# Optimization experiments

Measured on AMD Instinct MI355X. Metric: run time of the kernel, lower is better.

The kernel has to match this reference:

```python
import jax, jax.numpy as jnp
import numpy as np

N_NODES = 100000

def setup_inputs() -> dict:
    key = jax.random.key(0)
    k1, k2, k3, k4 = jax.random.split(key, 4)
    feat = jax.random.normal(k1, (N_NODES, 128), dtype=jnp.float32)
    weight = jax.random.normal(k2, (128, 64), dtype=jnp.float32) * 0.05
    src = jax.random.randint(k3, (600000,), 0, N_NODES, dtype=jnp.int64)
    dst = jax.random.randint(k4, (600000,), 0, N_NODES, dtype=jnp.int64)
    return {"feat": feat, "weight": weight, "src": src, "dst": dst}

def reference(feat, weight, src, dst):
    n = feat.shape[0]
    ones = jnp.ones(src.shape[0], dtype=jnp.float32)
    # out-degree of source nodes (edges leave src), in-degree of dst nodes
    out_deg = jnp.clip(jax.ops.segment_sum(ones, src, num_segments=n), 1.0)
    in_deg = jnp.clip(jax.ops.segment_sum(ones, dst, num_segments=n), 1.0)
    norm_src = (out_deg ** -0.5)[:, None]   # [N,1]
    norm_dst = (in_deg ** -0.5)[:, None]    # [N,1]
    # in_feats (128) > out_feats (64): project first, then aggregate
    h = jnp.matmul(feat, weight) * norm_src              # [N, 64]
    msgs = h[src]                                        # [E, 64] gather
    rst = jax.ops.segment_sum(msgs, dst, num_segments=n)  # [N, 64] scatter-sum
    rst = rst * norm_dst
    return rst
```

## Files before the change

kernel.cpp:

```cpp
#include <hip/hip_runtime.h>
#include <hip/hip_fp16.h>

#define IN_F 128
#define OUT_F 64
#define NB    256
#define BSH   9
#define CAP   3840
#define CHUNK 2048
#define KPF  136
#define KPW  144

using short8  = __attribute__((ext_vector_type(8))) short;
using float4v = __attribute__((ext_vector_type(4))) float;

static __device__ inline unsigned short f2bf(float x) {
    union { float f; unsigned u; } v; v.f = x;
    unsigned r = (v.u + 0x7fffu + ((v.u >> 16) & 1u)) >> 16;
    return (unsigned short)r;
}

__global__ __launch_bounds__(256) void bin_gemm_kernel(
    const int* __restrict__ src, const int* __restrict__ dst,
    int* __restrict__ gcur_d, int* __restrict__ gcur_s,
    unsigned* __restrict__ bkt_d, unsigned short* __restrict__ bkt_s,
    int E, int nbin,
    const float* __restrict__ feat, const float* __restrict__ W,
    __half* __restrict__ h, int n)
{
    __shared__ union {
        struct { int hd[NB]; int hs[NB]; int based[NB]; int bases[NB]; } bin;
        struct { unsigned short Fh[128 * KPF]; unsigned short Wt[64 * KPW]; } gm;
    } smem;

    const int tid = threadIdx.x;

    if (blockIdx.x < (unsigned)nbin) {
        const int e0 = blockIdx.x * CHUNK;

        smem.bin.hd[tid] = 0; smem.bin.hs[tid] = 0;
        __syncthreads();

        int sv[8], dv[8];
        #pragma unroll
        for (int j = 0; j < 8; ++j) {
            int i = e0 + j * 256 + tid;
            if (i < E) { sv[j] = src[i]; dv[j] = dst[i]; }
            else       { sv[j] = -1;     dv[j] = -1; }
        }
        #pragma unroll
        for (int j = 0; j < 8; ++j) {
            if (dv[j] >= 0) {
                atomicAdd(&smem.bin.hd[dv[j] >> BSH], 1);
                atomicAdd(&smem.bin.hs[sv[j] >> BSH], 1);
            }
        }
        __syncthreads();

        int cd = smem.bin.hd[tid], cs = smem.bin.hs[tid];
        smem.bin.based[tid] = cd ? atomicAdd(&gcur_d[tid], cd) : 0;
        smem.bin.bases[tid] = cs ? atomicAdd(&gcur_s[tid], cs) : 0;
        smem.bin.hd[tid] = 0; smem.bin.hs[tid] = 0;
        __syncthreads();

        #pragma unroll
        for (int j = 0; j < 8; ++j) {
            if (dv[j] >= 0) {
                int bd = dv[j] >> BSH;
                int pd = atomicAdd(&smem.bin.hd[bd], 1) + smem.bin.based[bd];
                if (pd < CAP)
                    bkt_d[(size_t)bd * CAP + pd] =
                        (unsigned)sv[j] | ((unsigned)(dv[j] & 511) << 17);
                int bs = sv[j] >> BSH;
                int ps = atomicAdd(&smem.bin.hs[bs], 1) + smem.bin.bases[bs];
                if (ps < CAP) bkt_s[(size_t)bs * CAP + ps] = (unsigned short)(sv[j] & 511);
            }
        }
        return;
    }

    unsigned short* Fh = smem.gm.Fh;
    unsigned short* Wt = smem.gm.Wt;
    const int row0 = (blockIdx.x - nbin) * 128;

    {
        const float4* W4 = (const float4*)W;
        #pragma unroll
        for (int it = 0; it < 8; ++it) {
            int i4 = it * 256 + tid;
            int k  = i4 >> 4;
            int c4 = (i4 & 15) * 4;
            float4 wv = W4[i4];
            Wt[(c4 + 0) * KPW + k] = f2bf(wv.x);
            Wt[(c4 + 1) * KPW + k] = f2bf(wv.y);
            Wt[(c4 + 2) * KPW + k] = f2bf(wv.z);
            Wt[(c4 + 3) * KPW + k] = f2bf(wv.w);
        }
    }
    {
        const float4* F4 = (const float4*)feat;
        #pragma unroll
        for (int it = 0; it < 16; ++it) {
            int i4 = it * 256 + tid;
            int r  = i4 >> 5;
            int c4 = (i4 & 31) * 4;
            int gr = row0 + r; if (gr >= n) gr = n - 1;
            float4 v = F4[(long)gr * 32 + (i4 & 31)];
            ushort4 u;
            u.x = f2bf(v.x); u.y = f2bf(v.y); u.z = f2bf(v.z); u.w = f2bf(v.w);
            *(ushort4*)&Fh[r * KPF + c4] = u;
        }
    }
    __syncthreads();

    const int w  = tid >> 6;
    const int l  = tid & 63;
    const int ml = l & 15;
    const int q  = l >> 4;

    float4v acc[2][4];
    #pragma unroll
    for (int rt = 0; rt < 2; ++rt)
        #pragma unroll
        for (int ct = 0; ct < 4; ++ct)
            acc[rt][ct] = (float4v){0.f, 0.f, 0.f, 0.f};

    #pragma unroll
    for (int ks = 0; ks < 4; ++ks) {
        const int ko = ks * 32 + q * 8;
        short8 a0 = *(const short8*)&Fh[(w * 32 +  0 + ml) * KPF + ko];
        short8 a1 = *(const short8*)&Fh[(w * 32 + 16 + ml) * KPF + ko];
        short8 b0 = *(const short8*)&Wt[( 0 + ml) * KPW + ko];
        short8 b1 = *(const short8*)&Wt[(16 + ml) * KPW + ko];
        short8 b2 = *(const short8*)&Wt[(32 + ml) * KPW + ko];
        short8 b3 = *(const short8*)&Wt[(48 + ml) * KPW + ko];
        acc[0][0] = __builtin_amdgcn_mfma_f32_16x16x32_bf16(a0, b0, acc[0][0], 0, 0, 0);
        acc[0][1] = __builtin_amdgcn_mfma_f32_16x16x32_bf16(a0, b1, acc[0][1], 0, 0, 0);
        acc[0][2] = __builtin_amdgcn_mfma_f32_16x16x32_bf16(a0, b2, acc[0][2], 0, 0, 0);
        acc[0][3] = __builtin_amdgcn_mfma_f32_16x16x32_bf16(a0, b3, acc[0][3], 0, 0, 0);
        acc[1][0] = __builtin_amdgcn_mfma_f32_16x16x32_bf16(a1, b0, acc[1][0], 0, 0, 0);
        acc[1][1] = __builtin_amdgcn_mfma_f32_16x16x32_bf16(a1, b1, acc[1][1], 0, 0, 0);
        acc[1][2] = __builtin_amdgcn_mfma_f32_16x16x32_bf16(a1, b2, acc[1][2], 0, 0, 0);
        acc[1][3] = __builtin_amdgcn_mfma_f32_16x16x32_bf16(a1, b3, acc[1][3], 0, 0, 0);
    }

    #pragma unroll
    for (int rt = 0; rt < 2; ++rt) {
        #pragma unroll
        for (int reg = 0; reg < 4; ++reg) {
            int row = row0 + w * 32 + rt * 16 + q * 4 + reg;
            if (row < n) {
                #pragma unroll
                for (int ct = 0; ct < 4; ++ct)
                    h[(long)row * OUT_F + ct * 16 + ml] = __float2half(acc[rt][ct][reg]);
            }
        }
    }
}

__global__ __launch_bounds__(256) void csr_kernel(
    const unsigned* __restrict__ bkt_d, const unsigned short* __restrict__ bkt_s,
    const int* __restrict__ gcur_d, const int* __restrict__ gcur_s,
    int2* __restrict__ off_deg, int* __restrict__ ebuf, int* __restrict__ outdeg, int n)
{
    __shared__ int hist[512], curs[512], hist_s[512];
    __shared__ int wsum[4];
    const int b = blockIdx.x, tid = threadIdx.x;
    const int cnt   = min(gcur_d[b], CAP);
    const int cnt_s = min(gcur_s[b], CAP);

    hist[tid] = 0; hist[tid + 256] = 0;
    hist_s[tid] = 0; hist_s[tid + 256] = 0;
    __syncthreads();

    unsigned rec[15];
    int nrec = 0;
    for (int i = tid; i < cnt; i += 256) {
        unsigned e = bkt_d[(size_t)b * CAP + i];
        rec[nrec++] = e;
        atomicAdd(&hist[e >> 17], 1);
    }
    for (int i = tid; i < cnt_s; i += 256)
        atomicAdd(&hist_s[bkt_s[(size_t)b * CAP + i]], 1);
    __syncthreads();

    int a0 = hist[2 * tid], a1 = hist[2 * tid + 1];
    int psum = a0 + a1;
    const int lane = tid & 63, w = tid >> 6;
    int x = psum;
    #pragma unroll
    for (int off = 1; off < 64; off <<= 1) {
        int y = __shfl_up(x, off);
        if (lane >= off) x += y;
    }
    if (lane == 63) wsum[w] = x;
    __syncthreads();
    int wbase = 0;
    for (int i = 0; i < w; ++i) wbase += wsum[i];
    int excl = x + wbase - psum;
    curs[2 * tid]     = excl;
    curs[2 * tid + 1] = excl + a0;
    off_deg[b * 512 + 2 * tid]     = make_int2(b * CAP + excl,      a0);
    off_deg[b * 512 + 2 * tid + 1] = make_int2(b * CAP + excl + a0, a1);
    __syncthreads();

    for (int j = 0; j < nrec; ++j) {
        unsigned e = rec[j];
        int p = atomicAdd(&curs[e >> 17], 1);
        if (p < CAP) ebuf[b * CAP + p] = (int)(e & 0x1FFFFu);
    }

    int node = b * 512 + tid;
    if (node < n) outdeg[node] = hist_s[tid];
    node += 256;
    if (node < n) outdeg[node] = hist_s[tid + 256];
}

__global__ __launch_bounds__(256) void gather_kernel(
    const int* __restrict__ ebuf, const int2* __restrict__ off_deg,
    const int* __restrict__ outdeg,
    const __half* __restrict__ h, float* __restrict__ out, int n)
{
    int d = blockIdx.x * 4 + (threadIdx.x >> 6);
    int l = threadIdx.x & 63;
    int o = l >> 3;
    int t = l & 7;
    if (d >= n) return;
    int2 od = off_deg[d];
    int beg = od.x, m = od.y, end = od.x + od.y;
    float a0 = 0.f, a1 = 0.f, a2 = 0.f, a3 = 0.f;
    float a4 = 0.f, a5 = 0.f, a6 = 0.f, a7 = 0.f;
    for (int j = beg + o; j < end; j += 8) {
        int s = ebuf[j];
        float ns = rsqrtf(fmaxf((float)outdeg[s], 1.0f));
        union { uint4 u; __half2 h2[4]; } P;
        P.u = *(const uint4*)&h[(long)s * OUT_F + 8 * t];
        float2 f0 = __half22float2(P.h2[0]);
        float2 f1 = __half22float2(P.h2[1]);
        float2 f2 = __half22float2(P.h2[2]);
        float2 f3 = __half22float2(P.h2[3]);
        a0 = fmaf(f0.x, ns, a0); a1 = fmaf(f0.y, ns, a1);
        a2 = fmaf(f1.x, ns, a2); a3 = fmaf(f1.y, ns, a3);
        a4 = fmaf(f2.x, ns, a4); a5 = fmaf(f2.y, ns, a5);
        a6 = fmaf(f3.x, ns, a6); a7 = fmaf(f3.y, ns, a7);
    }
    #pragma unroll
    for (int mask = 8; mask <= 32; mask <<= 1) {
        a0 += __shfl_xor(a0, mask); a1 += __shfl_xor(a1, mask);
        a2 += __shfl_xor(a2, mask); a3 += __shfl_xor(a3, mask);
        a4 += __shfl_xor(a4, mask); a5 += __shfl_xor(a5, mask);
        a6 += __shfl_xor(a6, mask); a7 += __shfl_xor(a7, mask);
    }
    if (o == 0) {
        float nd = rsqrtf(fmaxf((float)m, 1.0f));
        float4 v0 = make_float4(a0 * nd, a1 * nd, a2 * nd, a3 * nd);
        float4 v1 = make_float4(a4 * nd, a5 * nd, a6 * nd, a7 * nd);
        *(float4*)&out[(long)d * OUT_F + 8 * t]     = v0;
        *(float4*)&out[(long)d * OUT_F + 8 * t + 4] = v1;
    }
}

extern "C" void kernel_launch(void* const* d_in, const int* in_sizes, int n_in,
                              void* d_out, int out_size, void* d_ws, size_t ws_size,
                              hipStream_t stream) {
    const float* feat = (const float*)d_in[0];
    const float* W    = (const float*)d_in[1];
    const int*   src  = (const int*)d_in[2];
    const int*   dst  = (const int*)d_in[3];
    float* out = (float*)d_out;

    const int n = in_sizes[0] / IN_F;
    const int E = in_sizes[2];

    char* wsb = (char*)d_ws;
    int* gcur_d = (int*)wsb;
    int* gcur_s = gcur_d + NB;
    int* outdeg = gcur_s + NB;
    size_t pos = (((size_t)(2 * NB + n)) * 4 + 15) & ~(size_t)15;
    int2* off_deg = (int2*)(wsb + pos);
    pos = (pos + (size_t)NB * 512 * 8 + 15) & ~(size_t)15;
    int* ebuf = (int*)(wsb + pos);
    pos = (pos + (size_t)NB * CAP * 4 + 15) & ~(size_t)15;
    unsigned* bkt_d = (unsigned*)(wsb + pos);
    pos = (pos + (size_t)NB * CAP * 4 + 15) & ~(size_t)15;
    unsigned short* bkt_s = (unsigned short*)(wsb + pos);
    pos = (pos + (size_t)NB * CAP * 2 + 15) & ~(size_t)15;
    __half* h = (__half*)(wsb + pos);

    hipMemsetAsync(gcur_d, 0, 2 * NB * sizeof(int), stream);

    const int nbin  = (E + CHUNK - 1) / CHUNK;
    const int ngemm = (n + 127) / 128;

    bin_gemm_kernel<<<nbin + ngemm, 256, 0, stream>>>(src, dst, gcur_d, gcur_s,
                                                      bkt_d, bkt_s, E, nbin,
                                                      feat, W, h, n);
    csr_kernel<<<NB, 256, 0, stream>>>(bkt_d, bkt_s, gcur_d, gcur_s,
                                       off_deg, ebuf, outdeg, n);
    gather_kernel<<<(n + 3) / 4, 256, 0, stream>>>(ebuf, off_deg, outdeg, h, out, n);
}
```

Before: 155.9 us.

## Replace CSR build and per-node gather with per-bucket LDS atomic accumulation

Drops the CSR construction (histogram, scan, edge scatter into ebuf) and the per-destination gather kernel. Instead, each of 256 blocks processes its destination bucket directly and accumulates messages into a 512x65 float LDS tile with shared-memory atomics, then normalizes and writes out. Out-degree counting moves to a small separate kernel. This removes a global write and read pass plus a kernel's worth of work, at the cost of LDS atomic contention and only 256 blocks with ~133KB LDS each, which limits occupancy to one block per CU.

Measured after the change: 383.2 us. 146% more time.

```diff
diff --git a/kernel.cpp b/kernel.cpp
--- a/kernel.cpp
+++ b/kernel.cpp
@@ -9,6 +9,7 @@
 #define CHUNK 2048
 #define KPF  136
 #define KPW  144
+#define APITCH 65
 
 using short8  = __attribute__((ext_vector_type(8))) short;
 using float4v = __attribute__((ext_vector_type(4))) float;
@@ -157,80 +158,51 @@
     }
 }
 
-__global__ __launch_bounds__(256) void csr_kernel(
-    const unsigned* __restrict__ bkt_d, const unsigned short* __restrict__ bkt_s,
-    const int* __restrict__ gcur_d, const int* __restrict__ gcur_s,
-    int2* __restrict__ off_deg, int* __restrict__ ebuf, int* __restrict__ outdeg, int n)
+__global__ __launch_bounds__(256) void outdeg_kernel(
+    const unsigned short* __restrict__ bkt_s, const int* __restrict__ gcur_s,
+    int* __restrict__ outdeg, int n)
 {
-    __shared__ int hist[512], curs[512], hist_s[512];
-    __shared__ int wsum[4];
+    __shared__ int hs[512];
     const int b = blockIdx.x, tid = threadIdx.x;
-    const int cnt   = min(gcur_d[b], CAP);
     const int cnt_s = min(gcur_s[b], CAP);
 
-    hist[tid] = 0; hist[tid + 256] = 0;
-    hist_s[tid] = 0; hist_s[tid + 256] = 0;
-    __syncthreads();
-
-    unsigned rec[15];
-    int nrec = 0;
-    for (int i = tid; i < cnt; i += 256) {
-        unsigned e = bkt_d[(size_t)b * CAP + i];
-        rec[nrec++] = e;
-        atomicAdd(&hist[e >> 17], 1);
-    }
+    hs[tid] = 0; hs[tid + 256] = 0;
+    __syncthreads();
+
+    const unsigned short* bp = bkt_s + (size_t)b * CAP;
     for (int i = tid; i < cnt_s; i += 256)
-        atomicAdd(&hist_s[bkt_s[(size_t)b * CAP + i]], 1);
-    __syncthreads();
-
-    int a0 = hist[2 * tid], a1 = hist[2 * tid + 1];
-    int psum = a0 + a1;
-    const int lane = tid & 63, w = tid >> 6;
-    int x = psum;
-    #pragma unroll
-    for (int off = 1; off < 64; off <<= 1) {
-        int y = __shfl_up(x, off);
-        if (lane >= off) x += y;
-    }
-    if (lane == 63) wsum[w] = x;
-    __syncthreads();
-    int wbase = 0;
-    for (int i = 0; i < w; ++i) wbase += wsum[i];
-    int excl = x + wbase - psum;
-    curs[2 * tid]     = excl;
-    curs[2 * tid + 1] = excl + a0;
-    off_deg[b * 512 + 2 * tid]     = make_int2(b * CAP + excl,      a0);
-    off_deg[b * 512 + 2 * tid + 1] = make_int2(b * CAP + excl + a0, a1);
-    __syncthreads();
-
-    for (int j = 0; j < nrec; ++j) {
-        unsigned e = rec[j];
-        int p = atomicAdd(&curs[e >> 17], 1);
-        if (p < CAP) ebuf[b * CAP + p] = (int)(e & 0x1FFFFu);
-    }
+        atomicAdd(&hs[bp[i]], 1);
+    __syncthreads();
 
     int node = b * 512 + tid;
-    if (node < n) outdeg[node] = hist_s[tid];
+    if (node < n) outdeg[node] = hs[tid];
     node += 256;
-    if (node < n) outdeg[node] = hist_s[tid + 256];
-}
-
-__global__ __launch_bounds__(256) void gather_kernel(
-    const int* __restrict__ ebuf, const int2* __restrict__ off_deg,
+    if (node < n) outdeg[node] = hs[tid + 256];
+}
+
+__global__ __launch_bounds__(512) void bucket_gather_kernel(
+    const unsigned* __restrict__ bkt_d, const int* __restrict__ gcur_d,
     const int* __restrict__ outdeg,
     const __half* __restrict__ h, float* __restrict__ out, int n)
 {
-    int d = blockIdx.x * 4 + (threadIdx.x >> 6);
-    int l = threadIdx.x & 63;
-    int o = l >> 3;
-    int t = l & 7;
-    if (d >= n) return;
-    int2 od = off_deg[d];
-    int beg = od.x, m = od.y, end = od.x + od.y;
-    float a0 = 0.f, a1 = 0.f, a2 = 0.f, a3 = 0.f;
-    float a4 = 0.f, a5 = 0.f, a6 = 0.f, a7 = 0.f;
-    for (int j = beg + o; j < end; j += 8) {
-        int s = ebuf[j];
+    __shared__ float acc[512 * APITCH];
+    __shared__ int hist[512];
+    const int b = blockIdx.x, tid = threadIdx.x;
+    const int cnt = min(gcur_d[b], CAP);
+
+    for (int i = tid; i < 512 * APITCH; i += 512) acc[i] = 0.f;
+    hist[tid & 511] = 0;
+    __syncthreads();
+
+    const int o = tid >> 3;
+    const int t = tid & 7;
+    const unsigned* bp = bkt_d + (size_t)b * CAP;
+
+    for (int j = o; j < cnt; j += 64) {
+        unsigned e = bp[j];
+        int s  = (int)(e & 0x1FFFFu);
+        int dl = (int)(e >> 17);
+        if (t == 0) atomicAdd(&hist[dl], 1);
         float ns = rsqrtf(fmaxf((float)outdeg[s], 1.0f));
         union { uint4 u; __half2 h2[4]; } P;
         P.u = *(const uint4*)&h[(long)s * OUT_F + 8 * t];
@@ -238,24 +210,27 @@
         float2 f1 = __half22float2(P.h2[1]);
         float2 f2 = __half22float2(P.h2[2]);
         float2 f3 = __half22float2(P.h2[3]);
-        a0 = fmaf(f0.x, ns, a0); a1 = fmaf(f0.y, ns, a1);
-        a2 = fmaf(f1.x, ns, a2); a3 = fmaf(f1.y, ns, a3);
-        a4 = fmaf(f2.x, ns, a4); a5 = fmaf(f2.y, ns, a5);
-        a6 = fmaf(f3.x, ns, a6); a7 = fmaf(f3.y, ns, a7);
-    }
-    #pragma unroll
-    for (int mask = 8; mask <= 32; mask <<= 1) {
-        a0 += __shfl_xor(a0, mask); a1 += __shfl_xor(a1, mask);
-        a2 += __shfl_xor(a2, mask); a3 += __shfl_xor(a3, mask);
-        a4 += __shfl_xor(a4, mask); a5 += __shfl_xor(a5, mask);
-        a6 += __shfl_xor(a6, mask); a7 += __shfl_xor(a7, mask);
-    }
-    if (o == 0) {
-        float nd = rsqrtf(fmaxf((float)m, 1.0f));
-        float4 v0 = make_float4(a0 * nd, a1 * nd, a2 * nd, a3 * nd);
-        float4 v1 = make_float4(a4 * nd, a5 * nd, a6 * nd, a7 * nd);
-        *(float4*)&out[(long)d * OUT_F + 8 * t]     = v0;
-        *(float4*)&out[(long)d * OUT_F + 8 * t + 4] = v1;
+        float* ap = &acc[dl * APITCH + 8 * t];
+        atomicAdd(&ap[0], f0.x * ns); atomicAdd(&ap[1], f0.y * ns);
+        atomicAdd(&ap[2], f1.x * ns); atomicAdd(&ap[3], f1.y * ns);
+        atomicAdd(&ap[4], f2.x * ns); atomicAdd(&ap[5], f2.y * ns);
+        atomicAdd(&ap[6], f3.x * ns); atomicAdd(&ap[7], f3.y * ns);
+    }
+    __syncthreads();
+
+    #pragma unroll
+    for (int pass = 0; pass < 8; ++pass) {
+        int r = pass * 64 + (tid >> 3);
+        int node = b * 512 + r;
+        if (node < n) {
+            float nd = rsqrtf(fmaxf((float)hist[r], 1.0f));
+            const float* ap = &acc[r * APITCH + 8 * (tid & 7)];
+            float4 v0 = make_float4(ap[0] * nd, ap[1] * nd, ap[2] * nd, ap[3] * nd);
+            float4 v1 = make_float4(ap[4] * nd, ap[5] * nd, ap[6] * nd, ap[7] * nd);
+            float* op = &out[(long)node * OUT_F + 8 * (tid & 7)];
+            *(float4*)op       = v0;
+            *(float4*)(op + 4) = v1;
+        }
     }
 }
 
@@ -276,10 +251,6 @@
     int* gcur_s = gcur_d + NB;
     int* outdeg = gcur_s + NB;
     size_t pos = (((size_t)(2 * NB + n)) * 4 + 15) & ~(size_t)15;
-    int2* off_deg = (int2*)(wsb + pos);
-    pos = (pos + (size_t)NB * 512 * 8 + 15) & ~(size_t)15;
-    int* ebuf = (int*)(wsb + pos);
-    pos = (pos + (size_t)NB * CAP * 4 + 15) & ~(size_t)15;
     unsigned* bkt_d = (unsigned*)(wsb + pos);
     pos = (pos + (size_t)NB * CAP * 4 + 15) & ~(size_t)15;
     unsigned short* bkt_s = (unsigned short*)(wsb + pos);
@@ -294,7 +265,6 @@
     bin_gemm_kernel<<<nbin + ngemm, 256, 0, stream>>>(src, dst, gcur_d, gcur_s,
                                                       bkt_d, bkt_s, E, nbin,
                                                       feat, W, h, n);
-    csr_kernel<<<NB, 256, 0, stream>>>(bkt_d, bkt_s, gcur_d, gcur_s,
-                                       off_deg, ebuf, outdeg, n);
-    gather_kernel<<<(n + 3) / 4, 256, 0, stream>>>(ebuf, off_deg, outdeg, h, out, n);
-}
+    outdeg_kernel<<<NB, 256, 0, stream>>>(bkt_s, gcur_s, outdeg, n);
+    bucket_gather_kernel<<<NB, 512, 0, stream>>>(bkt_d, gcur_d, outdeg, h, out, n);
+}
```
